# Optimization experiments

Measured on AMD Instinct MI355X. Metric: run time of the kernel, lower is better.

Reference implementation:

```python
import jax, jax.numpy as jnp
import numpy as np

B, K, N, DIM, C_IN = 4, 2048, 4096, 3, 61
IN = DIM + C_IN        # 64, deepset input size
H1, H2 = 128, 128      # neighbor_xf hidden sizes
OUT = 64               # c_out // heads
HEADS = 4
EPS = 1e-5             # BatchNorm eps


def _lin(key, i, o):
    return jax.random.normal(key, (i, o), jnp.float32) * (1.0 / np.sqrt(i))


def setup_inputs() -> dict:
    key = jax.random.key(0)
    ks = jax.random.split(key, 12)
    return {
        "keys": jax.random.normal(ks[0], (B, K, DIM), jnp.float32),
        "points": jax.random.normal(ks[1], (B, N, DIM), jnp.float32),
        "feats": jax.random.normal(ks[2], (B, N, C_IN), jnp.float32),
        "nx_w1": _lin(ks[3], IN, H1), "nx_b1": jnp.zeros((H1,), jnp.float32),
        "nx_w2": _lin(ks[4], H1, H2), "nx_b2": jnp.zeros((H2,), jnp.float32),
        "nx_w3": _lin(ks[5], H2, OUT), "nx_b3": jnp.zeros((OUT,), jnp.float32),
        "sx_w1": _lin(ks[6], IN, IN), "sx_b1": jnp.zeros((IN,), jnp.float32),
        "sx_w2": _lin(ks[7], IN, IN), "sx_b2": jnp.zeros((IN,), jnp.float32),
        "sx_w3": _lin(ks[8], IN, IN), "sx_b3": jnp.zeros((IN,), jnp.float32),
        "att_w": _lin(ks[9], 2 * IN, HEADS * IN),
        "att_b": jnp.zeros((HEADS * IN,), jnp.float32),
        "att_q": jax.random.normal(ks[10], (HEADS, IN), jnp.float32) * 0.1,
        "bn_gamma": jnp.ones((IN,), jnp.float32),
        "bn_beta": jnp.zeros((IN,), jnp.float32),
        "neighbors": 32,
    }


def _mlp3(x, w1, b1, w2, b2, w3, b3):
    # per-element deepset MLP: Linear-ReLU-Linear-ReLU-Linear
    h = jax.nn.relu(x @ w1 + b1)
    h = jax.nn.relu(h @ w2 + b2)
    return h @ w3 + b3


def _forward(keys, points, feats, nx_w1, nx_b1, nx_w2, nx_b2, nx_w3, nx_b3,
             sx_w1, sx_b1, sx_w2, sx_b2, sx_w3, sx_b3,
             att_w, att_b, att_q, bn_gamma, bn_beta, neighbors):
    b = keys.shape[0]
    # Euclidean dist_fn: dist_vec [B,K,N,dim], dist [B,K,N], all points valid
    rel = points[:, None, :, :] - keys[:, :, None, :]
    dist = jnp.sqrt(jnp.sum(rel * rel, axis=-1))
    _, idx = jax.lax.top_k(-dist, neighbors)                   # [B,K,k] nearest
    nrel = jnp.take_along_axis(rel, idx[..., None], axis=2)    # [B,K,k,dim]
    bidx = jnp.arange(b)[:, None, None]
    nfeat = feats[bidx, idx]                                   # [B,K,k,c_in]
    comb = jnp.concatenate([nrel, nfeat], axis=-1)             # [B,K,k,in]
    lat = _mlp3(comb, nx_w1, nx_b1, nx_w2, nx_b2, nx_w3, nx_b3)  # [B,K,k,out]
    # BatchNorm1d (training-mode batch stats) over flattened [B*K*k, in]
    flat = comb.reshape(-1, comb.shape[-1])
    mean = jnp.mean(flat, axis=0)
    var = jnp.var(flat, axis=0)
    norm = (comb - mean) * jax.lax.rsqrt(var + EPS) * bn_gamma + bn_beta
    # SelfAttention: deepset sum-pooled context + per-neighbor softmax weights
    set_feat = jnp.sum(_mlp3(norm, sx_w1, sx_b1, sx_w2, sx_b2, sx_w3, sx_b3), axis=2)
    comb_feat = jnp.concatenate(
        [norm, jnp.broadcast_to(set_feat[:, :, None, :], norm.shape)], axis=-1)
    heads = (comb_feat @ att_w + att_b).reshape(comb_feat.shape[:3] + (HEADS, -1))
    e = jnp.sum(heads * att_q, axis=-1)                        # [B,K,k,H]
    w = jax.nn.softmax(e, axis=-2)                             # softmax over neighbor axis
    out = jnp.einsum('bkno,bknh->bkoh', lat, w)                # weighted reduce over k
    return out.reshape(out.shape[:2] + (-1,))                  # [B,K,out*H]


def reference(keys, points, feats, nx_w1, nx_b1, nx_w2, nx_b2, nx_w3, nx_b3,
              sx_w1, sx_b1, sx_w2, sx_b2, sx_w3, sx_b3,
              att_w, att_b, att_q, bn_gamma, bn_beta, neighbors):
    return _forward(keys, points, feats, nx_w1, nx_b1, nx_w2, nx_b2, nx_w3, nx_b3,
                    sx_w1, sx_b1, sx_w2, sx_b2, sx_w3, sx_b3,
                    att_w, att_b, att_q, bn_gamma, bn_beta, neighbors)
```

## Files before the change

### kernel.cpp

```cpp
#include <hip/hip_runtime.h>
#include <math.h>

#define BATCH 4
#define KQ    2048
#define NPTS  4096
#define CIN   61
#define KNN   32
#define ROWS  (BATCH*KQ*KNN)

#define OFF_IDX  0
#define OFF_ACC  524288
#define OFF_ATTA 557056
#define OFF_W1F  558080
#define OFF_W2F  574464
#define OFF_W3F  607232

typedef __attribute__((ext_vector_type(8)))  short bfrag;
typedef __attribute__((ext_vector_type(4)))  unsigned ufrag;
typedef __attribute__((ext_vector_type(16))) float cfrag;

__device__ __forceinline__ unsigned short bf16_rne(float x) {
  unsigned u = __float_as_uint(x);
  unsigned r = u + 0x7fffu + ((u >> 16) & 1u);
  return (unsigned short)(r >> 16);
}
__device__ __forceinline__ float4 ld4u(const float* p) {
  float4 r; __builtin_memcpy(&r, p, 16); return r;
}
__device__ __forceinline__ unsigned cvtpk(float lo, float hi) {
  unsigned r;
  asm("v_cvt_pk_bf16_f32 %0, %1, %2" : "=v"(r) : "v"(lo), "v"(hi));
  return r;
}
__device__ __forceinline__ float up_lo(unsigned pk) { return __uint_as_float(pk << 16); }
__device__ __forceinline__ float up_hi(unsigned pk) { return __uint_as_float(pk & 0xffff0000u); }

__device__ __forceinline__ cfrag zero16() {
  cfrag z;
#pragma unroll
  for (int i = 0; i < 16; ++i) z[i] = 0.f;
  return z;
}
__device__ __forceinline__ cfrag mfma_bu(bfrag a, ufrag b, cfrag c) {
  return __builtin_amdgcn_mfma_f32_32x32x16_bf16(a, __builtin_bit_cast(bfrag, b), c, 0, 0, 0);
}
__device__ __forceinline__ cfrag mfma_ub(ufrag a, bfrag b, cfrag c) {
  return __builtin_amdgcn_mfma_f32_32x32x16_bf16(__builtin_bit_cast(bfrag, a), b, c, 0, 0, 0);
}
__device__ __forceinline__ cfrag mfma_uu(ufrag a, ufrag b, cfrag c) {
  return __builtin_amdgcn_mfma_f32_32x32x16_bf16(__builtin_bit_cast(bfrag, a), __builtin_bit_cast(bfrag, b), c, 0, 0, 0);
}

#define NCAND 320

template<int NS>
__device__ __forceinline__ void select_emit(
    const unsigned* __restrict__ VAL, const int* __restrict__ IDXL,
    int mcount, unsigned hib, unsigned lob, int lane,
    const float* __restrict__ Pb, float kx, float ky, float kz,
    unsigned short* __restrict__ dst, int* __restrict__ SEL,
    float* __restrict__ accs) {
  const unsigned long long lmask = (1ull << lane) - 1ull;
  unsigned e[NS];
#pragma unroll
  for (int s = 0; s < NS; ++s) {
    int ei = s*64 + lane;
    e[s] = (ei < mcount) ? VAL[ei] : 0xffffffffu;
  }
  unsigned lo2 = lob, hi2 = hib;
  while (lo2 < hi2) {
    unsigned mid = lo2 + ((hi2 - lo2) >> 1);
    int c = 0;
#pragma unroll
    for (int s = 0; s < NS; ++s) c += (int)__popcll(__ballot(e[s] <= mid));
    if (c == KNN) { hi2 = mid; break; }
    if (c > KNN) hi2 = mid; else lo2 = mid + 1;
  }
  const unsigned T = hi2;
  float r0=0.f,r1=0.f,r2=0.f,r3=0.f,r4=0.f,r5=0.f;
  int base2 = 0;
#pragma unroll
  for (int s = 0; s < NS; ++s) {
    bool p = (e[s] <= T);
    unsigned long long m = __ballot(p);
    if (p) {
      int pos = base2 + (int)__popcll(m & lmask);
      if (pos < KNN) {
        int n = IDXL[s*64 + lane];
        SEL[pos] = n;
        dst[pos] = (unsigned short)n;
        float dx = Pb[n*3+0]-kx, dy = Pb[n*3+1]-ky, dz = Pb[n*3+2]-kz;
        r0 += dx; r1 += dy; r2 += dz;
        r3 += dx*dx; r4 += dy*dy; r5 += dz*dz;
      }
    }
    base2 += (int)__popcll(m);
  }
#pragma unroll
  for (int off = 32; off > 0; off >>= 1) {
    r0 += __shfl_down(r0, off); r1 += __shfl_down(r1, off);
    r2 += __shfl_down(r2, off); r3 += __shfl_down(r3, off);
    r4 += __shfl_down(r4, off); r5 += __shfl_down(r5, off);
  }
  if (lane == 0) {
    atomicAdd(&accs[0], r0); atomicAdd(&accs[1], r1); atomicAdd(&accs[2], r2);
    atomicAdd(&accs[64], r3); atomicAdd(&accs[65], r4); atomicAdd(&accs[66], r5);
  }
}

__device__ __forceinline__ void dispatch_select(
    const unsigned* VAL, const int* IDXL, int mcount, unsigned hib, unsigned lob,
    int lane, const float* Pb, float kx, float ky, float kz,
    unsigned short* dst, int* SEL, float* accs) {
  if (mcount <= 64)
    select_emit<1>(VAL, IDXL, mcount, hib, lob, lane, Pb, kx, ky, kz, dst, SEL, accs);
  else if (mcount <= 128)
    select_emit<2>(VAL, IDXL, mcount, hib, lob, lane, Pb, kx, ky, kz, dst, SEL, accs);
  else
    select_emit<5>(VAL, IDXL, mcount, hib, lob, lane, Pb, kx, ky, kz, dst, SEL, accs);
}

__global__ __launch_bounds__(256, 6) void topk_kernel(
    const float* __restrict__ keys, const float* __restrict__ points,
    const float* __restrict__ feats,
    const float* __restrict__ w1, const float* __restrict__ w2,
    const float* __restrict__ w3,
    const float* __restrict__ att_w, const float* __restrict__ att_q,
    unsigned short* __restrict__ idx_out, float* __restrict__ acc,
    short* __restrict__ w1f, short* __restrict__ w2f, short* __restrict__ w3f,
    float* __restrict__ attA) {
  if (blockIdx.x >= 4096) {
    const int bb = blockIdx.x - 4096;
    if (bb == 128) {
      const int t = threadIdx.x, c = t >> 2, h = t & 3;
      float s = 0.f;
      for (int d = 0; d < 64; ++d) s += att_w[c*256 + h*64 + d] * att_q[h*64 + d];
      attA[c*4 + h] = s;
      return;
    }
    int t = bb * 256 + threadIdx.x;
    if (t < 8192) {
      int j = t & 7, lane = (t >> 3) & 63, tk = t >> 9;
      int kc = tk & 3, tile = tk >> 2;
      int nh = tile*32 + (lane & 31), k = kc*16 + (lane >> 5)*8 + j;
      w1f[t] = (short)bf16_rne(w1[k*128 + nh]);
    } else if (t < 24576) {
      int t2 = t - 8192;
      int j = t2 & 7, lane = (t2 >> 3) & 63, tk = t2 >> 9;
      int kc = tk & 7, tile = tk >> 3;
      int nh = tile*32 + (lane & 31);
      int k = 32*(kc>>1) + 16*(kc&1) + 4*(lane>>5) + (j&3) + 8*(j>>2);
      w2f[t2] = (short)bf16_rne(w2[k*128 + nh]);
    } else {
      int t3 = t - 24576;
      int j = t3 & 7, lane = (t3 >> 3) & 63, tk = t3 >> 9;
      int kc = tk & 7, tile = tk >> 3;
      int nh = tile*32 + (lane & 31);
      int k = 32*(kc>>1) + 16*(kc&1) + 4*(lane>>5) + (j&3) + 8*(j>>2);
      w3f[t3] = (short)bf16_rne(w3[k*64 + nh]);
    }
    return;
  }

  __shared__ unsigned VAL[2][NCAND];
  __shared__ int IDXL[2][NCAND];
  __shared__ int SEL[2][KNN];
  __shared__ unsigned HIW[2][4], LOW[2][4];
  __shared__ int WTOT[2][4];
  __shared__ float FRED[64*33];
  __shared__ float FQ[64*33];
  const int tid = threadIdx.x;
  const int lane = tid & 63, wid = tid >> 6;
  const int g0 = blockIdx.x * 2, g1 = g0 + 1;
  const int b = g0 >> 11;
  const float kxA = keys[(size_t)g0*3+0], kyA = keys[(size_t)g0*3+1], kzA = keys[(size_t)g0*3+2];
  const float kxB = keys[(size_t)g1*3+0], kyB = keys[(size_t)g1*3+1], kzB = keys[(size_t)g1*3+2];
  const float* __restrict__ Pb = points + (size_t)b * NPTS * 3;

  unsigned uA[16], uB[16];
  unsigned lminA = 0xffffffffu, lminB = 0xffffffffu;
#pragma unroll
  for (int c4 = 0; c4 < 4; ++c4) {
    const float* pp = Pb + (size_t)(tid*16 + c4*4) * 3;
    float4 A = ld4u(pp), B4 = ld4u(pp + 4), C4 = ld4u(pp + 8);
    float x, y, z, dx, dy, dz;
#define DPT(slot, PX, PY, PZ)                                        \
    x = PX; y = PY; z = PZ;                                          \
    dx = x-kxA; dy = y-kyA; dz = z-kzA;                              \
    uA[slot] = __float_as_uint(dx*dx + dy*dy + dz*dz);               \
    lminA = min(lminA, uA[slot]);                                    \
    dx = x-kxB; dy = y-kyB; dz = z-kzB;                              \
    uB[slot] = __float_as_uint(dx*dx + dy*dy + dz*dz);               \
    lminB = min(lminB, uB[slot]);
    DPT(c4*4+0, A.x,  A.y,  A.z)
    DPT(c4*4+1, A.w,  B4.x, B4.y)
    DPT(c4*4+2, B4.z, B4.w, C4.x)
    DPT(c4*4+3, C4.y, C4.z, C4.w)
#undef DPT
  }
  unsigned wloA = lminA, whiA = lminA, wloB = lminB, whiB = lminB;
#pragma unroll
  for (int off = 1; off < 64; off <<= 1) {
    unsigned a0 = (unsigned)__shfl_xor((int)wloA, off);
    unsigned a1 = (unsigned)__shfl_xor((int)whiA, off);
    unsigned b0 = (unsigned)__shfl_xor((int)wloB, off);
    unsigned b1 = (unsigned)__shfl_xor((int)whiB, off);
    wloA = min(wloA, a0); whiA = max(whiA, a1);
    wloB = min(wloB, b0); whiB = max(whiB, b1);
  }
  unsigned hiA, hiB;
  {
    unsigned lo = wloA, hi = whiA;
    while (lo < hi) {
      unsigned mid = lo + ((hi - lo) >> 1);
      int c = (int)__popcll(__ballot(lminA <= mid));
      if (c == KNN) { hi = mid; break; }
      if (c > KNN) hi = mid; else lo = mid + 1;
    }
    hiA = hi;
    lo = wloB; hi = whiB;
    while (lo < hi) {
      unsigned mid = lo + ((hi - lo) >> 1);
      int c = (int)__popcll(__ballot(lminB <= mid));
      if (c == KNN) { hi = mid; break; }
      if (c > KNN) hi = mid; else lo = mid + 1;
    }
    hiB = hi;
  }
  if (lane == 0) {
    HIW[0][wid] = hiA; HIW[1][wid] = hiB;
    LOW[0][wid] = wloA; LOW[1][wid] = wloB;
  }
  __syncthreads();
  const unsigned hibA = min(min(HIW[0][0],HIW[0][1]), min(HIW[0][2],HIW[0][3]));
  const unsigned hibB = min(min(HIW[1][0],HIW[1][1]), min(HIW[1][2],HIW[1][3]));
  const unsigned lobA = min(min(LOW[0][0],LOW[0][1]), min(LOW[0][2],LOW[0][3]));
  const unsigned lobB = min(min(LOW[1][0],LOW[1][1]), min(LOW[1][2],LOW[1][3]));

  int cntA = 0, cntB = 0;
#pragma unroll
  for (int j = 0; j < 16; ++j) {
    cntA += (uA[j] <= hibA) ? 1 : 0;
    cntB += (uB[j] <= hibB) ? 1 : 0;
  }
  int incA = cntA, incB = cntB;
#pragma unroll
  for (int off = 1; off < 64; off <<= 1) {
    int tA = __shfl_up(incA, off);
    int tB = __shfl_up(incB, off);
    if (lane >= off) { incA += tA; incB += tB; }
  }
  if (lane == 63) { WTOT[0][wid] = incA; WTOT[1][wid] = incB; }
  __syncthreads();
  int baseA = incA - cntA, baseB = incB - cntB;
  for (int w = 0; w < wid; ++w) { baseA += WTOT[0][w]; baseB += WTOT[1][w]; }
  {
    int pA = baseA, pB = baseB;
#pragma unroll
    for (int j = 0; j < 16; ++j) {
      if (uA[j] <= hibA) {
        if (pA < NCAND) { VAL[0][pA] = uA[j]; IDXL[0][pA] = tid*16 + j; }
        ++pA;
      }
      if (uB[j] <= hibB) {
        if (pB < NCAND) { VAL[1][pB] = uB[j]; IDXL[1][pB] = tid*16 + j; }
        ++pB;
      }
    }
  }
  __syncthreads();
  const int mcountA = min(WTOT[0][0]+WTOT[0][1]+WTOT[0][2]+WTOT[0][3], NCAND);
  const int mcountB = min(WTOT[1][0]+WTOT[1][1]+WTOT[1][2]+WTOT[1][3], NCAND);

  float* accs = &acc[(blockIdx.x & 63)*128];
  if (wid == 0) {
    dispatch_select(VAL[0], IDXL[0], mcountA, hibA, lobA, lane, Pb,
                    kxA, kyA, kzA, idx_out + (size_t)g0*KNN, SEL[0], accs);
  } else if (wid == 2) {
    dispatch_select(VAL[1], IDXL[1], mcountB, hibB, lobB, lane, Pb,
                    kxB, kyB, kzB, idx_out + (size_t)g1*KNN, SEL[1], accs);
  }
  __syncthreads();

  {
    const int row = tid >> 3, chunk = tid & 7;
    const int nA = SEL[0][row], nB = SEL[1][row];
    const float* frA = feats + ((size_t)b*NPTS + nA)*CIN;
    const float* frB = feats + ((size_t)b*NPTS + nB)*CIN;
    float fs[8] = {0,0,0,0,0,0,0,0}, fq[8] = {0,0,0,0,0,0,0,0};
    if (chunk < 7) {
      float4 a0 = ld4u(frA + chunk*8), a1 = ld4u(frA + chunk*8 + 4);
      float4 b0 = ld4u(frB + chunk*8), b1 = ld4u(frB + chunk*8 + 4);
      fs[0]=a0.x+b0.x; fq[0]=a0.x*a0.x+b0.x*b0.x;
      fs[1]=a0.y+b0.y; fq[1]=a0.y*a0.y+b0.y*b0.y;
      fs[2]=a0.z+b0.z; fq[2]=a0.z*a0.z+b0.z*b0.z;
      fs[3]=a0.w+b0.w; fq[3]=a0.w*a0.w+b0.w*b0.w;
      fs[4]=a1.x+b1.x; fq[4]=a1.x*a1.x+b1.x*b1.x;
      fs[5]=a1.y+b1.y; fq[5]=a1.y*a1.y+b1.y*b1.y;
      fs[6]=a1.z+b1.z; fq[6]=a1.z*a1.z+b1.z*b1.z;
      fs[7]=a1.w+b1.w; fq[7]=a1.w*a1.w+b1.w*b1.w;
    } else {
#pragma unroll
      for (int i = 0; i < 5; ++i) {
        float va = frA[56+i], vb = frB[56+i];
        fs[i] = va + vb; fq[i] = va*va + vb*vb;
      }
    }
#pragma unroll
    for (int i = 0; i < 8; ++i) {
      FRED[(chunk*8 + i)*33 + row] = fs[i];
      FQ  [(chunk*8 + i)*33 + row] = fq[i];
    }
  }
  __syncthreads();
  if (tid < 64) {
    float s = 0.f, q2 = 0.f;
#pragma unroll
    for (int r = 0; r < 32; ++r) {
      s  += FRED[tid*33 + r];
      q2 += FQ[tid*33 + r];
    }
    if (tid < CIN) {
      atomicAdd(&accs[3 + tid], s);
      atomicAdd(&accs[64 + 3 + tid], q2);
    }
  }
}

#define L_W1F 0
#define L_W2F 16384
#define L_W3F 49152
#define L_SH  65536
#define L_SL  69632
#define L_B1  73728
#define L_B2  74240
#define L_B3  74752
#define L_WSC 75008
#define L_SC  79104
#define L_TOT 79360

__global__ __launch_bounds__(512, 4) void main_kernel(
    const float* __restrict__ keys, const float* __restrict__ points,
    const float* __restrict__ feats, const unsigned short* __restrict__ idxg,
    const short* __restrict__ w1f, const short* __restrict__ w2f,
    const short* __restrict__ w3f,
    const float* __restrict__ b1, const float* __restrict__ b2,
    const float* __restrict__ b3,
    const float* __restrict__ attAg, const float* __restrict__ accg,
    const float* __restrict__ gammav, float* __restrict__ out) {
  __shared__ __align__(16) char smem[L_TOT];
  const int tid = threadIdx.x;
  const int bid = blockIdx.x;
  const int wid = tid >> 6, lane = tid & 63;
  const int col = lane & 31, h = lane >> 5;

  {
    const uint4* src = (const uint4*)w1f;
    uint4* dst = (uint4*)smem;
#pragma unroll
    for (int r = 0; r < 8; ++r) dst[r*512 + tid] = src[r*512 + tid];
    if (tid < 128) ((float*)(smem + L_B1))[tid] = b1[tid];
    else if (tid < 256) ((float*)(smem + L_B2))[tid-128] = b2[tid-128];
    else if (tid < 320) ((float*)(smem + L_B3))[tid-256] = b3[tid-256];
    float* TMP = (float*)(smem + L_WSC);
    {
      int c = tid & 63, p = tid >> 6;
      float s = 0.f, s2 = 0.f;
      for (int k = p; k < 64; k += 8) {
        s += accg[k*128 + c]; s2 += accg[k*128 + 64 + c];
      }
      TMP[p*128 + c] = s; TMP[p*128 + 64 + c] = s2;
    }
    __syncthreads();
    float* SCp = (float*)(smem + L_SC);
    if (tid < 64) {
      float s = 0.f, s2 = 0.f;
#pragma unroll
      for (int p = 0; p < 8; ++p) { s += TMP[p*128 + tid]; s2 += TMP[p*128 + 64 + tid]; }
      const float invR = 1.f / (float)ROWS;
      float mean = s * invR;
      float var = s2 * invR - mean * mean;
      SCp[tid] = gammav[tid] * rsqrtf(var + 1e-5f);
    }
    __syncthreads();
    {
      const int s = tid >> 8;
      const int kc = (tid >> 6) & 3;
      const int ln = tid & 63;
      const int hd = ln & 31;
      short* dstf = (short*)(smem + (s ? L_SL : L_SH)) + (kc*64 + ln)*8;
#pragma unroll
      for (int j = 0; j < 8; ++j) {
        const int ch = kc*16 + (ln>>5)*8 + j;
        float val = (hd < 4) ? attAg[ch*4 + hd] * SCp[ch] : 0.f;
        unsigned hb = bf16_rne(val);
        if (s) {
          float lo = val - __uint_as_float(hb << 16);
          dstf[j] = (short)bf16_rne(lo);
        } else {
          dstf[j] = (short)hb;
        }
      }
    }
    __syncthreads();
  }

  float* WS = (float*)(smem + L_WSC) + wid*128;
  const short* SW1 = (const short*)(smem + L_W1F);
  const short* SW2 = (const short*)(smem + L_W2F);
  const short* SW3 = (const short*)(smem + L_W3F);
  const float* SB1 = (const float*)(smem + L_B1);
  const float* SB2 = (const float*)(smem + L_B2);

  for (int qi = 0; qi < 2; ++qi) {
    const int g = bid*8 + wid + qi*4096;
    const int b = g >> 11;
    const int n = (int)idxg[(size_t)g*KNN + col];
    const float* frow = feats + ((size_t)b*NPTS + n)*CIN;

    float v[4][8];
    if (h == 0) {
      const float* Pb = points + (size_t)b*NPTS*3;
      v[0][0] = Pb[n*3+0] - keys[(size_t)g*3+0];
      v[0][1] = Pb[n*3+1] - keys[(size_t)g*3+1];
      v[0][2] = Pb[n*3+2] - keys[(size_t)g*3+2];
      float4 t0 = ld4u(frow);
      v[0][3]=t0.x; v[0][4]=t0.y; v[0][5]=t0.z; v[0][6]=t0.w;
      v[0][7] = frow[4];
    } else {
      float4 a0 = ld4u(frow+5), a1 = ld4u(frow+9);
      v[0][0]=a0.x; v[0][1]=a0.y; v[0][2]=a0.z; v[0][3]=a0.w;
      v[0][4]=a1.x; v[0][5]=a1.y; v[0][6]=a1.z; v[0][7]=a1.w;
    }
#pragma unroll
    for (int kc = 1; kc < 4; ++kc) {
      const int f0 = kc*16 + 8*h - 3;
      float4 a0 = ld4u(frow+f0), a1 = ld4u(frow+f0+4);
      v[kc][0]=a0.x; v[kc][1]=a0.y; v[kc][2]=a0.z; v[kc][3]=a0.w;
      v[kc][4]=a1.x; v[kc][5]=a1.y; v[kc][6]=a1.z; v[kc][7]=a1.w;
    }

    ufrag ahi[4], alo[4];
#pragma unroll
    for (int kc = 0; kc < 4; ++kc)
#pragma unroll
      for (int p = 0; p < 4; ++p) {
        unsigned pk = cvtpk(v[kc][2*p], v[kc][2*p+1]);
        ahi[kc][p] = pk;
        alo[kc][p] = cvtpk(v[kc][2*p] - up_lo(pk), v[kc][2*p+1] - up_hi(pk));
      }

    cfrag Ef = zero16();
#pragma unroll
    for (int kc = 0; kc < 4; ++kc) {
      bfrag sh = *(const bfrag*)((const short*)(smem + L_SH) + (kc*64 + lane)*8);
      bfrag sl = *(const bfrag*)((const short*)(smem + L_SL) + (kc*64 + lane)*8);
      Ef = mfma_ub(ahi[kc], sh, Ef);
      Ef = mfma_ub(alo[kc], sh, Ef);
      Ef = mfma_ub(ahi[kc], sl, Ef);
    }

    float mx = Ef[0];
#pragma unroll
    for (int i = 1; i < 16; ++i) mx = fmaxf(mx, Ef[i]);
    mx = fmaxf(mx, __shfl_xor(mx, 32));
    float wsm[16], ssum = 0.f;
#pragma unroll
    for (int i = 0; i < 16; ++i) { wsm[i] = __expf(Ef[i] - mx); ssum += wsm[i]; }
    ssum += __shfl_xor(ssum, 32);
    const float invs = 1.f / ssum;
#pragma unroll
    for (int i = 0; i < 16; ++i) wsm[i] *= invs;

    if (col < 4) {
#pragma unroll
      for (int i = 0; i < 8; ++i) {
        const int c0 = (2*i & 3) + 8*(i >> 1);
        const int nA = c0 + 4*h;
        WS[nA*4 + col]     = wsm[2*i];
        WS[nA*4 + 4 + col] = wsm[2*i+1];
      }
    }
    const int hdc = col & 3;
    ufrag whi[2], wlo[2];
#pragma unroll
    for (int bb = 0; bb < 2; ++bb)
#pragma unroll
      for (int p = 0; p < 4; ++p) {
        const int c0 = (2*p & 3) + 8*(p >> 1);
        const int n0 = 16*bb + 4*h + c0;
        float r0 = WS[n0*4 + hdc], r1 = WS[n0*4 + 4 + hdc];
        unsigned pk = cvtpk(r0, r1);
        whi[bb][p] = pk;
        wlo[bb][p] = cvtpk(r0 - up_lo(pk), r1 - up_hi(pk));
      }

    ufrag a2[8];
#pragma unroll
    for (int t = 0; t < 4; ++t) {
      cfrag acc = zero16();
#pragma unroll
      for (int kc = 0; kc < 4; ++kc) {
        bfrag wf = *(const bfrag*)(SW1 + ((t*4 + kc)*64 + lane)*8);
        acc = mfma_bu(wf, ahi[kc], acc);
      }
#pragma unroll
      for (int i = 0; i < 8; ++i) {
        const int c0 = (2*i & 3) + 8*(i >> 1);
        float2 bb2 = *(const float2*)(SB1 + t*32 + c0 + 4*h);
        float x0 = fmaxf(acc[2*i]   + bb2.x, 0.f);
        float x1 = fmaxf(acc[2*i+1] + bb2.y, 0.f);
        a2[2*t + (i>>2)][i&3] = cvtpk(x0, x1);
      }
    }

    ufrag a3[8];
#pragma unroll
    for (int t = 0; t < 4; ++t) {
      cfrag acc = zero16();
#pragma unroll
      for (int kc = 0; kc < 8; ++kc) {
        bfrag wf = *(const bfrag*)(SW2 + ((t*8 + kc)*64 + lane)*8);
        acc = mfma_bu(wf, a2[kc], acc);
      }
#pragma unroll
      for (int i = 0; i < 8; ++i) {
        const int c0 = (2*i & 3) + 8*(i >> 1);
        float2 bb2 = *(const float2*)(SB2 + t*32 + c0 + 4*h);
        float x0 = fmaxf(acc[2*i]   + bb2.x, 0.f);
        float x1 = fmaxf(acc[2*i+1] + bb2.y, 0.f);
        a3[2*t + (i>>2)][i&3] = cvtpk(x0, x1);
      }
    }

#pragma unroll
    for (int t = 0; t < 2; ++t) {
      cfrag acc = zero16();
#pragma unroll
      for (int kc = 0; kc < 8; ++kc) {
        bfrag wf = *(const bfrag*)(SW3 + ((t*8 + kc)*64 + lane)*8);
        acc = mfma_ub(a3[kc], wf, acc);
      }
      const float bz = ((const float*)(smem + L_B3))[t*32 + col];
#pragma unroll
      for (int i = 0; i < 16; ++i) acc[i] += bz;
      ufrag lh[2], ll[2];
#pragma unroll
      for (int i = 0; i < 8; ++i) {
        unsigned pk = cvtpk(acc[2*i], acc[2*i+1]);
        lh[i>>2][i&3] = pk;
        ll[i>>2][i&3] = cvtpk(acc[2*i] - up_lo(pk), acc[2*i+1] - up_hi(pk));
      }
      cfrag og = zero16();
#pragma unroll
      for (int bb = 0; bb < 2; ++bb) og = mfma_uu(lh[bb], whi[bb], og);
#pragma unroll
      for (int bb = 0; bb < 2; ++bb) og = mfma_uu(ll[bb], whi[bb], og);
#pragma unroll
      for (int bb = 0; bb < 2; ++bb) og = mfma_uu(lh[bb], wlo[bb], og);
      if (col < 4) {
        float* op = out + (size_t)g*256 + t*128 + col;
#pragma unroll
        for (int i = 0; i < 16; ++i) {
          const int orow = (i&3) + 8*(i>>2) + 4*h;
          op[orow*4] = og[i];
        }
      }
    }
  }
}

extern "C" void kernel_launch(void* const* d_in, const int* in_sizes, int n_in,
                              void* d_out, int out_size, void* d_ws, size_t ws_size,
                              hipStream_t stream) {
  const float* keys   = (const float*)d_in[0];
  const float* points = (const float*)d_in[1];
  const float* feats  = (const float*)d_in[2];
  const float* nx_w1  = (const float*)d_in[3];
  const float* nx_b1  = (const float*)d_in[4];
  const float* nx_w2  = (const float*)d_in[5];
  const float* nx_b2  = (const float*)d_in[6];
  const float* nx_w3  = (const float*)d_in[7];
  const float* nx_b3  = (const float*)d_in[8];
  const float* att_w  = (const float*)d_in[15];
  const float* att_q  = (const float*)d_in[17];
  const float* gamma  = (const float*)d_in[18];
  float* out = (float*)d_out;

  char* ws = (char*)d_ws;
  unsigned short* idxp = (unsigned short*)(ws + OFF_IDX);
  float* acc  = (float*)(ws + OFF_ACC);
  float* attA = (float*)(ws + OFF_ATTA);
  short* w1f  = (short*)(ws + OFF_W1F);
  short* w2f  = (short*)(ws + OFF_W2F);
  short* w3f  = (short*)(ws + OFF_W3F);

  hipMemsetAsync(acc, 0, 32768, stream);
  topk_kernel<<<4096 + 129, 256, 0, stream>>>(keys, points, feats,
      nx_w1, nx_w2, nx_w3, att_w, att_q, idxp, acc, w1f, w2f, w3f, attA);
  main_kernel<<<512, 512, 0, stream>>>(keys, points, feats, idxp,
      w1f, w2f, w3f, nx_b1, nx_b2, nx_b3, attA, acc, gamma, out);
}
```

Baseline: 167.1 us.

## Process four queries per top-k block with per-wave threshold search

Each top-k block now handles four query keys instead of two, so each point tile is loaded once and reused for four distance computations. The grid is halved and launch bounds are lowered to 4 blocks per CU. Each wave now runs the threshold binary search for one query using only its own lanes' minima rather than combining all waves. That bound is looser, so the candidate buffer grows to 384 and a 3-slot select path is added. The neighbor-feature statistics are summed over four queries per block. Risks are more candidates to select per query, higher register and LDS pressure, and a search lower bound taken from one wave's minimum rather than the block's.

Measured after the change: 162.0 us. 1.03x faster.

```diff
diff --git a/kernel.cpp b/kernel.cpp
--- a/kernel.cpp
+++ b/kernel.cpp
@@ -51,7 +51,7 @@
   return __builtin_amdgcn_mfma_f32_32x32x16_bf16(__builtin_bit_cast(bfrag, a), __builtin_bit_cast(bfrag, b), c, 0, 0, 0);
 }
 
-#define NCAND 320
+#define NCAND 384
 
 template<int NS>
 __device__ __forceinline__ void select_emit(
@@ -116,11 +116,13 @@
     select_emit<1>(VAL, IDXL, mcount, hib, lob, lane, Pb, kx, ky, kz, dst, SEL, accs);
   else if (mcount <= 128)
     select_emit<2>(VAL, IDXL, mcount, hib, lob, lane, Pb, kx, ky, kz, dst, SEL, accs);
+  else if (mcount <= 192)
+    select_emit<3>(VAL, IDXL, mcount, hib, lob, lane, Pb, kx, ky, kz, dst, SEL, accs);
   else
-    select_emit<5>(VAL, IDXL, mcount, hib, lob, lane, Pb, kx, ky, kz, dst, SEL, accs);
-}
-
-__global__ __launch_bounds__(256, 6) void topk_kernel(
+    select_emit<6>(VAL, IDXL, mcount, hib, lob, lane, Pb, kx, ky, kz, dst, SEL, accs);
+}
+
+__global__ __launch_bounds__(256, 4) void topk_kernel(
     const float* __restrict__ keys, const float* __restrict__ points,
     const float* __restrict__ feats,
     const float* __restrict__ w1, const float* __restrict__ w2,
@@ -129,8 +131,8 @@
     unsigned short* __restrict__ idx_out, float* __restrict__ acc,
     short* __restrict__ w1f, short* __restrict__ w2f, short* __restrict__ w3f,
     float* __restrict__ attA) {
-  if (blockIdx.x >= 4096) {
-    const int bb = blockIdx.x - 4096;
+  if (blockIdx.x >= 2048) {
+    const int bb = blockIdx.x - 2048;
     if (bb == 128) {
       const int t = threadIdx.x, c = t >> 2, h = t & 3;
       float s = 0.f;
@@ -162,23 +164,28 @@
     return;
   }
 
-  __shared__ unsigned VAL[2][NCAND];
-  __shared__ int IDXL[2][NCAND];
-  __shared__ int SEL[2][KNN];
-  __shared__ unsigned HIW[2][4], LOW[2][4];
-  __shared__ int WTOT[2][4];
+  __shared__ unsigned VAL[4][NCAND];
+  __shared__ int IDXL[4][NCAND];
+  __shared__ int SEL[4][KNN];
+  __shared__ unsigned HIB[4];
+  __shared__ int WTOT[4][4];
   __shared__ float FRED[64*33];
   __shared__ float FQ[64*33];
   const int tid = threadIdx.x;
   const int lane = tid & 63, wid = tid >> 6;
-  const int g0 = blockIdx.x * 2, g1 = g0 + 1;
+  const int g0 = blockIdx.x * 4;
   const int b = g0 >> 11;
-  const float kxA = keys[(size_t)g0*3+0], kyA = keys[(size_t)g0*3+1], kzA = keys[(size_t)g0*3+2];
-  const float kxB = keys[(size_t)g1*3+0], kyB = keys[(size_t)g1*3+1], kzB = keys[(size_t)g1*3+2];
+  float4 K0 = ld4u(keys + (size_t)g0*3);
+  float4 K1 = ld4u(keys + (size_t)g0*3 + 4);
+  float4 K2 = ld4u(keys + (size_t)g0*3 + 8);
+  const float kx0=K0.x, ky0=K0.y, kz0=K0.z;
+  const float kx1=K0.w, ky1=K1.x, kz1=K1.y;
+  const float kx2=K1.z, ky2=K1.w, kz2=K2.x;
+  const float kx3=K2.y, ky3=K2.z, kz3=K2.w;
   const float* __restrict__ Pb = points + (size_t)b * NPTS * 3;
 
-  unsigned uA[16], uB[16];
-  unsigned lminA = 0xffffffffu, lminB = 0xffffffffu;
+  unsigned u0[16], u1[16], u2[16], u3[16];
+  unsigned lm0 = 0xffffffffu, lm1 = 0xffffffffu, lm2 = 0xffffffffu, lm3 = 0xffffffffu;
 #pragma unroll
   for (int c4 = 0; c4 < 4; ++c4) {
     const float* pp = Pb + (size_t)(tid*16 + c4*4) * 3;
@@ -186,124 +193,116 @@
     float x, y, z, dx, dy, dz;
 #define DPT(slot, PX, PY, PZ)                                        \
     x = PX; y = PY; z = PZ;                                          \
-    dx = x-kxA; dy = y-kyA; dz = z-kzA;                              \
-    uA[slot] = __float_as_uint(dx*dx + dy*dy + dz*dz);               \
-    lminA = min(lminA, uA[slot]);                                    \
-    dx = x-kxB; dy = y-kyB; dz = z-kzB;                              \
-    uB[slot] = __float_as_uint(dx*dx + dy*dy + dz*dz);               \
-    lminB = min(lminB, uB[slot]);
+    dx = x-kx0; dy = y-ky0; dz = z-kz0;                              \
+    u0[slot] = __float_as_uint(dx*dx + dy*dy + dz*dz);               \
+    lm0 = min(lm0, u0[slot]);                                        \
+    dx = x-kx1; dy = y-ky1; dz = z-kz1;                              \
+    u1[slot] = __float_as_uint(dx*dx + dy*dy + dz*dz);               \
+    lm1 = min(lm1, u1[slot]);                                        \
+    dx = x-kx2; dy = y-ky2; dz = z-kz2;                              \
+    u2[slot] = __float_as_uint(dx*dx + dy*dy + dz*dz);               \
+    lm2 = min(lm2, u2[slot]);                                        \
+    dx = x-kx3; dy = y-ky3; dz = z-kz3;                              \
+    u3[slot] = __float_as_uint(dx*dx + dy*dy + dz*dz);               \
+    lm3 = min(lm3, u3[slot]);
     DPT(c4*4+0, A.x,  A.y,  A.z)
     DPT(c4*4+1, A.w,  B4.x, B4.y)
     DPT(c4*4+2, B4.z, B4.w, C4.x)
     DPT(c4*4+3, C4.y, C4.z, C4.w)
 #undef DPT
   }
-  unsigned wloA = lminA, whiA = lminA, wloB = lminB, whiB = lminB;
+
+  const unsigned lmw = (wid == 0) ? lm0 : (wid == 1) ? lm1 : (wid == 2) ? lm2 : lm3;
+  unsigned wlo = lmw, whi = lmw;
 #pragma unroll
   for (int off = 1; off < 64; off <<= 1) {
-    unsigned a0 = (unsigned)__shfl_xor((int)wloA, off);
-    unsigned a1 = (unsigned)__shfl_xor((int)whiA, off);
-    unsigned b0 = (unsigned)__shfl_xor((int)wloB, off);
-    unsigned b1 = (unsigned)__shfl_xor((int)whiB, off);
-    wloA = min(wloA, a0); whiA = max(whiA, a1);
-    wloB = min(wloB, b0); whiB = max(whiB, b1);
-  }
-  unsigned hiA, hiB;
+    unsigned a0 = (unsigned)__shfl_xor((int)wlo, off);
+    unsigned a1 = (unsigned)__shfl_xor((int)whi, off);
+    wlo = min(wlo, a0); whi = max(whi, a1);
+  }
   {
-    unsigned lo = wloA, hi = whiA;
+    unsigned lo = wlo, hi = whi;
     while (lo < hi) {
       unsigned mid = lo + ((hi - lo) >> 1);
-      int c = (int)__popcll(__ballot(lminA <= mid));
+      int c = (int)__popcll(__ballot(lmw <= mid));
       if (c == KNN) { hi = mid; break; }
       if (c > KNN) hi = mid; else lo = mid + 1;
     }
-    hiA = hi;
-    lo = wloB; hi = whiB;
-    while (lo < hi) {
-      unsigned mid = lo + ((hi - lo) >> 1);
-      int c = (int)__popcll(__ballot(lminB <= mid));
-      if (c == KNN) { hi = mid; break; }
-      if (c > KNN) hi = mid; else lo = mid + 1;
-    }
-    hiB = hi;
-  }
-  if (lane == 0) {
-    HIW[0][wid] = hiA; HIW[1][wid] = hiB;
-    LOW[0][wid] = wloA; LOW[1][wid] = wloB;
+    if (lane == 0) HIB[wid] = hi;
   }
   __syncthreads();
-  const unsigned hibA = min(min(HIW[0][0],HIW[0][1]), min(HIW[0][2],HIW[0][3]));
-  const unsigned hibB = min(min(HIW[1][0],HIW[1][1]), min(HIW[1][2],HIW[1][3]));
-  const unsigned lobA = min(min(LOW[0][0],LOW[0][1]), min(LOW[0][2],LOW[0][3]));
-  const unsigned lobB = min(min(LOW[1][0],LOW[1][1]), min(LOW[1][2],LOW[1][3]));
-
-  int cntA = 0, cntB = 0;
+  const unsigned hb0 = HIB[0], hb1 = HIB[1], hb2 = HIB[2], hb3 = HIB[3];
+
+  int c0 = 0, c1 = 0, c2 = 0, c3 = 0;
 #pragma unroll
   for (int j = 0; j < 16; ++j) {
-    cntA += (uA[j] <= hibA) ? 1 : 0;
-    cntB += (uB[j] <= hibB) ? 1 : 0;
-  }
-  int incA = cntA, incB = cntB;
+    c0 += (u0[j] <= hb0) ? 1 : 0;
+    c1 += (u1[j] <= hb1) ? 1 : 0;
+    c2 += (u2[j] <= hb2) ? 1 : 0;
+    c3 += (u3[j] <= hb3) ? 1 : 0;
+  }
+  int i0 = c0, i1 = c1, i2 = c2, i3 = c3;
 #pragma unroll
   for (int off = 1; off < 64; off <<= 1) {
-    int tA = __shfl_up(incA, off);
-    int tB = __shfl_up(incB, off);
-    if (lane >= off) { incA += tA; incB += tB; }
-  }
-  if (lane == 63) { WTOT[0][wid] = incA; WTOT[1][wid] = incB; }
+    int t0 = __shfl_up(i0, off), t1 = __shfl_up(i1, off);
+    int t2 = __shfl_up(i2, off), t3 = __shfl_up(i3, off);
+    if (lane >= off) { i0 += t0; i1 += t1; i2 += t2; i3 += t3; }
+  }
+  if (lane == 63) {
+    WTOT[0][wid] = i0; WTOT[1][wid] = i1; WTOT[2][wid] = i2; WTOT[3][wid] = i3;
+  }
   __syncthreads();
-  int baseA = incA - cntA, baseB = incB - cntB;
-  for (int w = 0; w < wid; ++w) { baseA += WTOT[0][w]; baseB += WTOT[1][w]; }
+  int p0 = i0 - c0, p1 = i1 - c1, p2 = i2 - c2, p3 = i3 - c3;
+  for (int w = 0; w < wid; ++w) {
+    p0 += WTOT[0][w]; p1 += WTOT[1][w]; p2 += WTOT[2][w]; p3 += WTOT[3][w];
+  }
+#pragma unroll
+  for (int j = 0; j < 16; ++j) {
+    const int n = tid*16 + j;
+    if (u0[j] <= hb0) { if (p0 < NCAND) { VAL[0][p0] = u0[j]; IDXL[0][p0] = n; } ++p0; }
+    if (u1[j] <= hb1) { if (p1 < NCAND) { VAL[1][p1] = u1[j]; IDXL[1][p1] = n; } ++p1; }
+    if (u2[j] <= hb2) { if (p2 < NCAND) { VAL[2][p2] = u2[j]; IDXL[2][p2] = n; } ++p2; }
+    if (u3[j] <= hb3) { if (p3 < NCAND) { VAL[3][p3] = u3[j]; IDXL[3][p3] = n; } ++p3; }
+  }
+  __syncthreads();
+
+  float* accs = &acc[(blockIdx.x & 63)*128];
   {
-    int pA = baseA, pB = baseB;
-#pragma unroll
-    for (int j = 0; j < 16; ++j) {
-      if (uA[j] <= hibA) {
-        if (pA < NCAND) { VAL[0][pA] = uA[j]; IDXL[0][pA] = tid*16 + j; }
-        ++pA;
-      }
-      if (uB[j] <= hibB) {
-        if (pB < NCAND) { VAL[1][pB] = uB[j]; IDXL[1][pB] = tid*16 + j; }
-        ++pB;
-      }
-    }
-  }
-  __syncthreads();
-  const int mcountA = min(WTOT[0][0]+WTOT[0][1]+WTOT[0][2]+WTOT[0][3], NCAND);
-  const int mcountB = min(WTOT[1][0]+WTOT[1][1]+WTOT[1][2]+WTOT[1][3], NCAND);
-
-  float* accs = &acc[(blockIdx.x & 63)*128];
-  if (wid == 0) {
-    dispatch_select(VAL[0], IDXL[0], mcountA, hibA, lobA, lane, Pb,
-                    kxA, kyA, kzA, idx_out + (size_t)g0*KNN, SEL[0], accs);
-  } else if (wid == 2) {
-    dispatch_select(VAL[1], IDXL[1], mcountB, hibB, lobB, lane, Pb,
-                    kxB, kyB, kzB, idx_out + (size_t)g1*KNN, SEL[1], accs);
+    const int mcount = min(WTOT[wid][0]+WTOT[wid][1]+WTOT[wid][2]+WTOT[wid][3], NCAND);
+    const unsigned hibw = (wid == 0) ? hb0 : (wid == 1) ? hb1 : (wid == 2) ? hb2 : hb3;
+    const float kxw = (wid == 0) ? kx0 : (wid == 1) ? kx1 : (wid == 2) ? kx2 : kx3;
+    const float kyw = (wid == 0) ? ky0 : (wid == 1) ? ky1 : (wid == 2) ? ky2 : ky3;
+    const float kzw = (wid == 0) ? kz0 : (wid == 1) ? kz1 : (wid == 2) ? kz2 : kz3;
+    dispatch_select(VAL[wid], IDXL[wid], mcount, hibw, wlo, lane, Pb,
+                    kxw, kyw, kzw, idx_out + (size_t)(g0 + wid)*KNN, SEL[wid], accs);
   }
   __syncthreads();
 
   {
     const int row = tid >> 3, chunk = tid & 7;
     const int nA = SEL[0][row], nB = SEL[1][row];
+    const int nC = SEL[2][row], nD = SEL[3][row];
     const float* frA = feats + ((size_t)b*NPTS + nA)*CIN;
     const float* frB = feats + ((size_t)b*NPTS + nB)*CIN;
+    const float* frC = feats + ((size_t)b*NPTS + nC)*CIN;
+    const float* frD = feats + ((size_t)b*NPTS + nD)*CIN;
     float fs[8] = {0,0,0,0,0,0,0,0}, fq[8] = {0,0,0,0,0,0,0,0};
     if (chunk < 7) {
-      float4 a0 = ld4u(frA + chunk*8), a1 = ld4u(frA + chunk*8 + 4);
-      float4 b0 = ld4u(frB + chunk*8), b1 = ld4u(frB + chunk*8 + 4);
-      fs[0]=a0.x+b0.x; fq[0]=a0.x*a0.x+b0.x*b0.x;
-      fs[1]=a0.y+b0.y; fq[1]=a0.y*a0.y+b0.y*b0.y;
-      fs[2]=a0.z+b0.z; fq[2]=a0.z*a0.z+b0.z*b0.z;
-      fs[3]=a0.w+b0.w; fq[3]=a0.w*a0.w+b0.w*b0.w;
-      fs[4]=a1.x+b1.x; fq[4]=a1.x*a1.x+b1.x*b1.x;
-      fs[5]=a1.y+b1.y; fq[5]=a1.y*a1.y+b1.y*b1.y;
-      fs[6]=a1.z+b1.z; fq[6]=a1.z*a1.z+b1.z*b1.z;
-      fs[7]=a1.w+b1.w; fq[7]=a1.w*a1.w+b1.w*b1.w;
+      const float* fr[4] = {frA, frB, frC, frD};
+#pragma unroll
+      for (int qq = 0; qq < 4; ++qq) {
+        float4 a0 = ld4u(fr[qq] + chunk*8), a1 = ld4u(fr[qq] + chunk*8 + 4);
+        fs[0]+=a0.x; fq[0]+=a0.x*a0.x; fs[1]+=a0.y; fq[1]+=a0.y*a0.y;
+        fs[2]+=a0.z; fq[2]+=a0.z*a0.z; fs[3]+=a0.w; fq[3]+=a0.w*a0.w;
+        fs[4]+=a1.x; fq[4]+=a1.x*a1.x; fs[5]+=a1.y; fq[5]+=a1.y*a1.y;
+        fs[6]+=a1.z; fq[6]+=a1.z*a1.z; fs[7]+=a1.w; fq[7]+=a1.w*a1.w;
+      }
     } else {
 #pragma unroll
       for (int i = 0; i < 5; ++i) {
-        float va = frA[56+i], vb = frB[56+i];
-        fs[i] = va + vb; fq[i] = va*va + vb*vb;
+        float va = frA[56+i], vb = frB[56+i], vc = frC[56+i], vd = frD[56+i];
+        fs[i] = va + vb + vc + vd;
+        fq[i] = va*va + vb*vb + vc*vc + vd*vd;
       }
     }
 #pragma unroll
@@ -596,7 +595,7 @@
   short* w3f  = (short*)(ws + OFF_W3F);
 
   hipMemsetAsync(acc, 0, 32768, stream);
-  topk_kernel<<<4096 + 129, 256, 0, stream>>>(keys, points, feats,
+  topk_kernel<<<2048 + 129, 256, 0, stream>>>(keys, points, feats,
       nx_w1, nx_w2, nx_w3, att_w, att_q, idxp, acc, w1f, w2f, w3f, attA);
   main_kernel<<<512, 512, 0, stream>>>(keys, points, feats, idxp,
       w1f, w2f, w3f, nx_b1, nx_b2, nx_b3, attA, acc, gamma, out);
```
